# Optimization experiments

Measured on AMD Instinct MI355X. Metric: run time of the kernel, lower is better.

Reference implementation:

```python
import jax, jax.numpy as jnp
import numpy as np

EMB = 64

def _segment_mean(x, ids, num_segments):
    s = jax.ops.segment_sum(x, ids, num_segments=num_segments)
    c = jax.ops.segment_sum(jnp.ones((ids.shape[0], 1), x.dtype), ids, num_segments=num_segments)
    return s / jnp.maximum(c, 1.0)

def setup_inputs() -> dict:
    key = jax.random.key(0)
    ks = jax.random.split(key, 8)
    E, N, G = 800000, 50000, 16
    edge_distance_vec = jax.random.normal(ks[0], (E, 3), dtype=jnp.float32)
    x_edge = jax.random.normal(ks[1], (E, EMB), dtype=jnp.float32)
    edge_index = jax.random.randint(ks[2], (E,), 0, N, dtype=jnp.int64)
    batch = jnp.sort(jax.random.randint(ks[3], (N,), 0, G, dtype=jnp.int64))
    # MLP params (torch Linear: y = x @ W.T + b); store as [in, out]
    lim1 = 1.0 / np.sqrt(EMB)
    W1 = jax.random.uniform(ks[4], (EMB, EMB), jnp.float32, -lim1, lim1)
    b1 = jax.random.uniform(ks[5], (EMB,), jnp.float32, -lim1, lim1)
    W2 = jax.random.uniform(ks[6], (EMB, 1), jnp.float32, -lim1, lim1)
    b2 = jax.random.uniform(ks[7], (1,), jnp.float32, -lim1, lim1)
    return {"edge_distance_vec": edge_distance_vec, "x_edge": x_edge,
            "edge_index": edge_index, "batch": batch,
            "n_nodes": N, "n_graphs": G,
            "W1": W1, "b1": b1, "W2": W2, "b2": b2}

def reference(edge_distance_vec, x_edge, edge_index, batch, n_nodes, n_graphs, W1, b1, W2, b2):
    E = edge_distance_vec.shape[0]
    # outer product of edge vectors -> [E, 9]
    outer = (edge_distance_vec[:, :, None] * edge_distance_vec[:, None, :]).reshape(E, 9)
    # edge_outer = x_edge[:, :, None] * outer[:, None, :] -> transpose(1,2) -> [E, 9, emb]
    edge_outer = outer[:, :, None] * x_edge[:, None, :]
    # per-edge, per-component MLP: Linear(emb,emb) -> SiLU -> Linear(emb,1)
    h = jax.nn.silu(jnp.einsum('eci,io->eco', edge_outer, W1) + b1)
    edge_out = (jnp.einsum('eci,io->eco', h, W2) + b2).reshape(E, 9)
    # scatter-mean edge -> node, then node -> graph (non-extensive)
    node_outer = _segment_mean(edge_out, edge_index, n_nodes)
    stress = _segment_mean(node_outer, batch, n_graphs)
    return stress
```

## Files before the change

kernel.cpp:

```cpp
#include <hip/hip_runtime.h>

#define EMB  64
#define NREP 256

typedef __attribute__((ext_vector_type(8))) short bf16x8;
typedef __attribute__((ext_vector_type(4))) float f32x4;
union BF8 { bf16x8 v; short s[8]; };

static __device__ __forceinline__ short f2bf(float f) {
    unsigned u = __float_as_uint(f);
    u += 0x7fffu + ((u >> 16) & 1u);
    return (short)(u >> 16);
}

__global__ __launch_bounds__(256) void prep_kernel(
    const int* __restrict__ eidx, int* __restrict__ ecnt, int E,
    const int* __restrict__ batch, int* __restrict__ gStart, int N)
{
    int t = blockIdx.x * 256 + threadIdx.x;
    if (t < N) {
        int g = batch[t];
        if (t == 0 || batch[t - 1] != g) gStart[g] = t;
    }
    if (t < E) atomicAdd(&ecnt[eidx[t]], 1);
}

__global__ __launch_bounds__(256, 4) void edge_kernel(
    const float* __restrict__ dvec, const float* __restrict__ x_edge,
    const int*   __restrict__ eidx, const int* __restrict__ batch,
    const int*   __restrict__ ecnt,
    const float* __restrict__ W1, const float* __restrict__ b1,
    const float* __restrict__ W2, const float* __restrict__ b2,
    float* __restrict__ repsum, int E)
{
    __shared__ float bins[96];
    __shared__ float sb1[64], sw2[64];
    const int tid = threadIdx.x;
    if (tid < 96) bins[tid] = 0.f;
    if (tid < 64) { sb1[tid] = b1[tid]; sw2[tid] = W2[tid]; }
    __syncthreads();

    const int lane = tid & 63, wave = tid >> 6;
    const int col  = lane & 15, quad = lane >> 4;

    BF8 Af[4][2];
    #pragma unroll
    for (int mt = 0; mt < 4; ++mt)
        #pragma unroll
        for (int kt = 0; kt < 2; ++kt) {
            const float* wp = W1 + (kt * 32 + quad * 8) * 64 + mt * 16 + col;
            #pragma unroll
            for (int j = 0; j < 8; ++j) Af[mt][kt].s[j] = f2bf(wp[j * 64]);
        }

    const float NL2E = -1.442695040888963f;
    const float bb2  = b2[0];
    const long  ebase = (long)blockIdx.x * 256 + wave * 64;

    #pragma unroll 1
    for (int nt = 0; nt < 4; ++nt) {
        long e = ebase + nt * 16 + col;
        bool valid = (e < E);
        if (!valid) e = 0;

        int   n = 0; float scale = 0.f; int g = 0;
        if (quad < 2) {
            n = eidx[e];
            scale = 1.0f / (float)max(ecnt[n], 1);
            g = batch[n];
        }

        const float* xp = x_edge + (size_t)e * EMB + quad * 8;
        f32x4 xa = *(const f32x4*)(xp);
        f32x4 xb = *(const f32x4*)(xp + 4);
        f32x4 xc = *(const f32x4*)(xp + 32);
        f32x4 xd = *(const f32x4*)(xp + 36);
        BF8 B0, B1;
        B0.s[0] = f2bf(xa.x); B0.s[1] = f2bf(xa.y); B0.s[2] = f2bf(xa.z); B0.s[3] = f2bf(xa.w);
        B0.s[4] = f2bf(xb.x); B0.s[5] = f2bf(xb.y); B0.s[6] = f2bf(xb.z); B0.s[7] = f2bf(xb.w);
        B1.s[0] = f2bf(xc.x); B1.s[1] = f2bf(xc.y); B1.s[2] = f2bf(xc.z); B1.s[3] = f2bf(xc.w);
        B1.s[4] = f2bf(xd.x); B1.s[5] = f2bf(xd.y); B1.s[6] = f2bf(xd.z); B1.s[7] = f2bf(xd.w);

        float d0 = dvec[3 * e + 0];
        float d1 = dvec[3 * e + 1];
        float d2 = dvec[3 * e + 2];
        float a[6] = { d0 * d0, d1 * d1, d2 * d2, d0 * d1, d0 * d2, d1 * d2 };

        float acc[6] = { 0.f, 0.f, 0.f, 0.f, 0.f, 0.f };

        #pragma unroll
        for (int mt = 0; mt < 4; ++mt) {
            f32x4 D = { 0.f, 0.f, 0.f, 0.f };
            D = __builtin_amdgcn_mfma_f32_16x16x32_bf16(Af[mt][0].v, B0.v, D, 0, 0, 0);
            D = __builtin_amdgcn_mfma_f32_16x16x32_bf16(Af[mt][1].v, B1.v, D, 0, 0, 0);
            #pragma unroll
            for (int r = 0; r < 4; ++r) {
                int   o  = mt * 16 + quad * 4 + r;
                float y  = D[r];
                float b  = sb1[o];
                float w2 = sw2[o];
                #pragma unroll
                for (int c = 0; c < 6; ++c) {
                    float z  = fmaf(a[c], y, b);
                    float ex = __builtin_amdgcn_exp2f(z * NL2E);
                    float rr = __builtin_amdgcn_rcpf(1.0f + ex);
                    acc[c]   = fmaf(w2, z * rr, acc[c]);
                }
            }
        }

        #pragma unroll
        for (int c = 0; c < 6; ++c) {
            acc[c] += __shfl_xor(acc[c], 16, 64);
            acc[c] += __shfl_xor(acc[c], 32, 64);
        }

        if (valid && quad < 2) {
            #pragma unroll
            for (int j = 0; j < 3; ++j) {
                int c = quad * 3 + j;
                atomicAdd(&bins[g * 6 + c], (acc[c] + bb2) * scale);
            }
        }
    }

    __syncthreads();
    if (tid < 96) {
        int rep = blockIdx.x & (NREP - 1);
        atomicAdd(repsum + (size_t)rep * 96 + tid, bins[tid]);
    }
}

__global__ __launch_bounds__(384) void final_kernel(
    const float* __restrict__ repsum, const int* __restrict__ gStart,
    float* __restrict__ out, int N)
{
    __shared__ float part[4][96];
    __shared__ float sh[96];
    __shared__ int gs[17];
    int t = threadIdx.x;
    int r0 = t / 96, gc = t % 96;
    float s = 0.f;
    #pragma unroll 8
    for (int r = r0; r < NREP; r += 4) s += repsum[(size_t)r * 96 + gc];
    part[r0][gc] = s;
    if (t == 0) {
        gs[16] = N;
        for (int g = 15; g >= 0; --g) {
            unsigned v = (unsigned)gStart[g];
            gs[g] = (v > (unsigned)gs[g + 1]) ? gs[g + 1] : (int)v;
        }
    }
    __syncthreads();
    if (t < 96) sh[t] = part[0][t] + part[1][t] + part[2][t] + part[3][t];
    __syncthreads();
    if (t < 16) {
        int gN = gs[t + 1] - gs[t];
        float inv = 1.0f / fmaxf((float)gN, 1.0f);
        float m0 = sh[t * 6 + 0] * inv;
        float m1 = sh[t * 6 + 1] * inv;
        float m2 = sh[t * 6 + 2] * inv;
        float m3 = sh[t * 6 + 3] * inv;
        float m4 = sh[t * 6 + 4] * inv;
        float m5 = sh[t * 6 + 5] * inv;
        float* p = out + t * 9;
        p[0] = m0; p[1] = m3; p[2] = m4;
        p[3] = m3; p[4] = m1; p[5] = m5;
        p[6] = m4; p[7] = m5; p[8] = m2;
    }
}

extern "C" void kernel_launch(void* const* d_in, const int* in_sizes, int n_in,
                              void* d_out, int out_size, void* d_ws, size_t ws_size,
                              hipStream_t stream) {
    const float* dvec   = (const float*)d_in[0];
    const float* x_edge = (const float*)d_in[1];
    const int*   eidx   = (const int*)d_in[2];
    const int*   batch  = (const int*)d_in[3];
    const float* W1     = (const float*)d_in[6];
    const float* b1     = (const float*)d_in[7];
    const float* W2     = (const float*)d_in[8];
    const float* b2     = (const float*)d_in[9];

    int E = in_sizes[0] / 3;
    int N = in_sizes[3];

    int*   ecnt   = (int*)d_ws;
    float* repsum = (float*)(ecnt + N);
    int*   gStart = (int*)(repsum + (size_t)NREP * 96);

    hipMemsetAsync(d_ws, 0, ((size_t)N + (size_t)NREP * 96) * 4, stream);
    hipMemsetAsync(gStart, 0xFF, 17 * 4, stream);

    int blocks = (E + 255) / 256;
    prep_kernel<<<blocks, 256, 0, stream>>>(eidx, ecnt, E, batch, gStart, N);
    edge_kernel<<<blocks, 256, 0, stream>>>(dvec, x_edge, eidx, batch, ecnt,
                                            W1, b1, W2, b2, repsum, E);
    final_kernel<<<1, 384, 0, stream>>>(repsum, gStart, (float*)d_out, N);
}
```

Baseline: 403.0 us.

## Software-pipeline edge loads and simplify SiLU math with packed bf16 convert

Unrolls the four edge tiles per wave into a two-stage software pipeline in which loads for the next tile are issued before the current tile's MFMA and SiLU work, hiding global memory latency. It also folds the -log2e factor and the b1*W2 product into shared-memory tables so the inner SiLU loop does fewer multiplies. Float-to-bf16 conversion now uses the packed v_cvt_pk_bf16_f32 instruction instead of manual rounding. The invalid-edge path is now handled by zeroing the scale rather than skipping the atomics, and double-buffered registers raise register pressure under the 4-blocks launch bound.

```diff
diff --git a/kernel.cpp b/kernel.cpp
--- a/kernel.cpp
+++ b/kernel.cpp
@@ -5,12 +5,18 @@
 
 typedef __attribute__((ext_vector_type(8))) short bf16x8;
 typedef __attribute__((ext_vector_type(4))) float f32x4;
-union BF8 { bf16x8 v; short s[8]; };
+union BF8 { bf16x8 v; short s[8]; unsigned u[4]; };
 
 static __device__ __forceinline__ short f2bf(float f) {
     unsigned u = __float_as_uint(f);
     u += 0x7fffu + ((u >> 16) & 1u);
     return (short)(u >> 16);
+}
+
+static __device__ __forceinline__ unsigned cvt2(float lo, float hi) {
+    unsigned r;
+    asm("v_cvt_pk_bf16_f32 %0, %1, %2" : "=v"(r) : "v"(lo), "v"(hi));
+    return r;
 }
 
 __global__ __launch_bounds__(256) void prep_kernel(
@@ -34,10 +40,16 @@
     float* __restrict__ repsum, int E)
 {
     __shared__ float bins[96];
-    __shared__ float sb1[64], sw2[64];
+    __shared__ float sb1N[64], sw2[64], sw2b[64];
     const int tid = threadIdx.x;
+    const float NL2E = -1.442695040888963f;
     if (tid < 96) bins[tid] = 0.f;
-    if (tid < 64) { sb1[tid] = b1[tid]; sw2[tid] = W2[tid]; }
+    if (tid < 64) {
+        float b = b1[tid], w = W2[tid];
+        sb1N[tid] = b * NL2E;
+        sw2[tid]  = w;
+        sw2b[tid] = w * b;
+    }
     __syncthreads();
 
     const int lane = tid & 63, wave = tid >> 6;
@@ -53,76 +65,95 @@
             for (int j = 0; j < 8; ++j) Af[mt][kt].s[j] = f2bf(wp[j * 64]);
         }
 
-    const float NL2E = -1.442695040888963f;
     const float bb2  = b2[0];
     const long  ebase = (long)blockIdx.x * 256 + wave * 64;
 
-    #pragma unroll 1
-    for (int nt = 0; nt < 4; ++nt) {
-        long e = ebase + nt * 16 + col;
-        bool valid = (e < E);
-        if (!valid) e = 0;
-
-        int   n = 0; float scale = 0.f; int g = 0;
-        if (quad < 2) {
-            n = eidx[e];
-            scale = 1.0f / (float)max(ecnt[n], 1);
-            g = batch[n];
-        }
-
-        const float* xp = x_edge + (size_t)e * EMB + quad * 8;
-        f32x4 xa = *(const f32x4*)(xp);
-        f32x4 xb = *(const f32x4*)(xp + 4);
-        f32x4 xc = *(const f32x4*)(xp + 32);
-        f32x4 xd = *(const f32x4*)(xp + 36);
-        BF8 B0, B1;
-        B0.s[0] = f2bf(xa.x); B0.s[1] = f2bf(xa.y); B0.s[2] = f2bf(xa.z); B0.s[3] = f2bf(xa.w);
-        B0.s[4] = f2bf(xb.x); B0.s[5] = f2bf(xb.y); B0.s[6] = f2bf(xb.z); B0.s[7] = f2bf(xb.w);
-        B1.s[0] = f2bf(xc.x); B1.s[1] = f2bf(xc.y); B1.s[2] = f2bf(xc.z); B1.s[3] = f2bf(xc.w);
-        B1.s[4] = f2bf(xd.x); B1.s[5] = f2bf(xd.y); B1.s[6] = f2bf(xd.z); B1.s[7] = f2bf(xd.w);
-
-        float d0 = dvec[3 * e + 0];
-        float d1 = dvec[3 * e + 1];
-        float d2 = dvec[3 * e + 2];
-        float a[6] = { d0 * d0, d1 * d1, d2 * d2, d0 * d1, d0 * d2, d1 * d2 };
-
-        float acc[6] = { 0.f, 0.f, 0.f, 0.f, 0.f, 0.f };
-
-        #pragma unroll
-        for (int mt = 0; mt < 4; ++mt) {
-            f32x4 D = { 0.f, 0.f, 0.f, 0.f };
-            D = __builtin_amdgcn_mfma_f32_16x16x32_bf16(Af[mt][0].v, B0.v, D, 0, 0, 0);
-            D = __builtin_amdgcn_mfma_f32_16x16x32_bf16(Af[mt][1].v, B1.v, D, 0, 0, 0);
-            #pragma unroll
-            for (int r = 0; r < 4; ++r) {
-                int   o  = mt * 16 + quad * 4 + r;
-                float y  = D[r];
-                float b  = sb1[o];
-                float w2 = sw2[o];
-                #pragma unroll
-                for (int c = 0; c < 6; ++c) {
-                    float z  = fmaf(a[c], y, b);
-                    float ex = __builtin_amdgcn_exp2f(z * NL2E);
-                    float rr = __builtin_amdgcn_rcpf(1.0f + ex);
-                    acc[c]   = fmaf(w2, z * rr, acc[c]);
-                }
-            }
-        }
-
-        #pragma unroll
-        for (int c = 0; c < 6; ++c) {
-            acc[c] += __shfl_xor(acc[c], 16, 64);
-            acc[c] += __shfl_xor(acc[c], 32, 64);
-        }
-
-        if (valid && quad < 2) {
-            #pragma unroll
-            for (int j = 0; j < 3; ++j) {
-                int c = quad * 3 + j;
-                atomicAdd(&bins[g * 6 + c], (acc[c] + bb2) * scale);
-            }
-        }
-    }
+#define PIPE_ISSUE(NT, XA, XB, XC, XD, DD0, DD1, DD2, NN, VM)                  \
+    {                                                                          \
+        long e_ = ebase + (NT) * 16 + col;                                     \
+        VM = (e_ < E);                                                         \
+        if (!VM) e_ = 0;                                                       \
+        const float* xp_ = x_edge + (size_t)e_ * EMB + quad * 8;               \
+        XA = *(const f32x4*)(xp_);                                             \
+        XB = *(const f32x4*)(xp_ + 4);                                         \
+        XC = *(const f32x4*)(xp_ + 32);                                        \
+        XD = *(const f32x4*)(xp_ + 36);                                        \
+        DD0 = dvec[3 * e_ + 0];                                                \
+        DD1 = dvec[3 * e_ + 1];                                                \
+        DD2 = dvec[3 * e_ + 2];                                                \
+        if (quad < 2) NN = eidx[e_];                                           \
+    }
+
+#define PIPE_BODY(XA, XB, XC, XD, DD0, DD1, DD2, NN, VM, PRE)                  \
+    {                                                                          \
+        float scale_ = 0.f; int g_ = 0;                                        \
+        if (quad < 2) {                                                        \
+            int cnt_ = max(ecnt[NN], 1);                                       \
+            g_ = batch[NN];                                                    \
+            scale_ = __builtin_amdgcn_rcpf((float)cnt_);                       \
+            if (!VM) scale_ = 0.f;                                             \
+        }                                                                      \
+        BF8 B0_, B1_;                                                          \
+        B0_.u[0] = cvt2(XA.x, XA.y); B0_.u[1] = cvt2(XA.z, XA.w);              \
+        B0_.u[2] = cvt2(XB.x, XB.y); B0_.u[3] = cvt2(XB.z, XB.w);              \
+        B1_.u[0] = cvt2(XC.x, XC.y); B1_.u[1] = cvt2(XC.z, XC.w);              \
+        B1_.u[2] = cvt2(XD.x, XD.y); B1_.u[3] = cvt2(XD.z, XD.w);              \
+        float a_[6] = { DD0*DD0, DD1*DD1, DD2*DD2, DD0*DD1, DD0*DD2, DD1*DD2 };\
+        float aN_[6];                                                          \
+        _Pragma("unroll")                                                      \
+        for (int c = 0; c < 6; ++c) aN_[c] = a_[c] * NL2E;                     \
+        PRE                                                                    \
+        float acc_[6] = { 0.f, 0.f, 0.f, 0.f, 0.f, 0.f };                      \
+        _Pragma("unroll")                                                      \
+        for (int mt = 0; mt < 4; ++mt) {                                       \
+            f32x4 D_ = { 0.f, 0.f, 0.f, 0.f };                                 \
+            D_ = __builtin_amdgcn_mfma_f32_16x16x32_bf16(Af[mt][0].v, B0_.v, D_, 0, 0, 0); \
+            D_ = __builtin_amdgcn_mfma_f32_16x16x32_bf16(Af[mt][1].v, B1_.v, D_, 0, 0, 0); \
+            _Pragma("unroll")                                                  \
+            for (int r = 0; r < 4; ++r) {                                      \
+                int   o_  = mt * 16 + quad * 4 + r;                            \
+                float y_  = D_[r];                                             \
+                float bN_ = sb1N[o_];                                          \
+                float wy_ = sw2[o_] * y_;                                      \
+                float wb_ = sw2b[o_];                                          \
+                _Pragma("unroll")                                              \
+                for (int c = 0; c < 6; ++c) {                                  \
+                    float arg_ = fmaf(aN_[c], y_, bN_);                        \
+                    float ex_  = __builtin_amdgcn_exp2f(arg_);                 \
+                    float rr_  = __builtin_amdgcn_rcpf(1.0f + ex_);            \
+                    float w2z_ = fmaf(a_[c], wy_, wb_);                        \
+                    acc_[c]    = fmaf(w2z_, rr_, acc_[c]);                     \
+                }                                                              \
+            }                                                                  \
+        }                                                                      \
+        _Pragma("unroll")                                                      \
+        for (int c = 0; c < 6; ++c) {                                          \
+            acc_[c] += __shfl_xor(acc_[c], 16, 64);                            \
+            acc_[c] += __shfl_xor(acc_[c], 32, 64);                            \
+        }                                                                      \
+        if (quad < 2) {                                                        \
+            _Pragma("unroll")                                                  \
+            for (int j = 0; j < 3; ++j) {                                      \
+                int c = quad * 3 + j;                                          \
+                atomicAdd(&bins[g_ * 6 + c], (acc_[c] + bb2) * scale_);        \
+            }                                                                  \
+        }                                                                      \
+    }
+
+    f32x4 Pxa, Pxb, Pxc, Pxd; float Pd0, Pd1, Pd2; int Pn = 0; bool Pv;
+    f32x4 Qxa, Qxb, Qxc, Qxd; float Qd0, Qd1, Qd2; int Qn = 0; bool Qv;
+
+    PIPE_ISSUE(0, Pxa, Pxb, Pxc, Pxd, Pd0, Pd1, Pd2, Pn, Pv)
+    PIPE_BODY(Pxa, Pxb, Pxc, Pxd, Pd0, Pd1, Pd2, Pn, Pv,
+              PIPE_ISSUE(1, Qxa, Qxb, Qxc, Qxd, Qd0, Qd1, Qd2, Qn, Qv))
+    PIPE_BODY(Qxa, Qxb, Qxc, Qxd, Qd0, Qd1, Qd2, Qn, Qv,
+              PIPE_ISSUE(2, Pxa, Pxb, Pxc, Pxd, Pd0, Pd1, Pd2, Pn, Pv))
+    PIPE_BODY(Pxa, Pxb, Pxc, Pxd, Pd0, Pd1, Pd2, Pn, Pv,
+              PIPE_ISSUE(3, Qxa, Qxb, Qxc, Qxd, Qd0, Qd1, Qd2, Qn, Qv))
+    PIPE_BODY(Qxa, Qxb, Qxc, Qxd, Qd0, Qd1, Qd2, Qn, Qv, )
+
+#undef PIPE_ISSUE
+#undef PIPE_BODY
 
     __syncthreads();
     if (tid < 96) {
```

After: 444.0 us. +10.2%, slower.
